# Kernel tuning notes

Measured on AMD Instinct MI355X. Metric: run time of the kernel, lower is better.

The kernel has to match this reference:

```python
import jax, jax.numpy as jnp
import numpy as np

NUM_HEADS = 16
B, S, D_MODEL = 8, 2048, 1024
HEAD_DIM = 64  # key_dim == value_dim == D_MODEL // NUM_HEADS


def setup_inputs() -> dict:
    key = jax.random.key(0)
    ks = jax.random.split(key, 8)
    s_in = 1.0 / np.sqrt(D_MODEL)
    s_out = 1.0 / np.sqrt(NUM_HEADS * HEAD_DIM)
    return {
        "query": jax.random.normal(ks[0], (B, S, D_MODEL), jnp.float32),
        "key": jax.random.normal(ks[1], (B, S, D_MODEL), jnp.float32),
        "value": jax.random.normal(ks[2], (B, S, D_MODEL), jnp.float32),
        "Wq": jax.random.normal(ks[3], (D_MODEL, HEAD_DIM), jnp.float32) * s_in,
        "bq": jnp.zeros((HEAD_DIM,), jnp.float32),
        "Wk": jax.random.normal(ks[4], (D_MODEL, HEAD_DIM), jnp.float32) * s_in,
        "bk": jnp.zeros((HEAD_DIM,), jnp.float32),
        "Wv": jax.random.normal(ks[5], (D_MODEL, HEAD_DIM), jnp.float32) * s_in,
        "bv": jnp.zeros((HEAD_DIM,), jnp.float32),
        "Wo": jax.random.normal(ks[6], (NUM_HEADS * HEAD_DIM, D_MODEL), jnp.float32) * s_out,
        "bo": jnp.zeros((D_MODEL,), jnp.float32),
    }


def reference(query, key, value, Wq, bq, Wk, bk, Wv, bv, Wo, bo):
    # Projections (same Linear reused for every "head" in the original code)
    q = query @ Wq + bq   # [B, S, head_dim]
    k = key @ Wk + bk     # [B, S, head_dim]
    v = value @ Wv + bv   # [B, S, head_dim]
    scale = jnp.sqrt(jnp.asarray(q.shape[-1], q.dtype))
    scores = jnp.einsum("bqd,bkd->bqk", q, k) / scale  # [B, S, S]
    attn = jax.nn.softmax(scores, axis=-1)
    ctx = jnp.einsum("bqk,bkd->bqd", attn, v)          # [B, S, head_dim]
    # All num_heads outputs are identical -> concat == tile
    cat = jnp.tile(ctx, (1, 1, NUM_HEADS))             # [B, S, num_heads*head_dim]
    return cat @ Wo + bo                               # [B, S, D_MODEL]
```

## Files before the change

### kernel.cpp

```cpp
#include <hip/hip_runtime.h>


typedef __attribute__((ext_vector_type(8))) unsigned short ushort8v;

__device__ __forceinline__ float bf2f(unsigned short u) {
    unsigned int x = ((unsigned int)u) << 16;
    return __builtin_bit_cast(float, x);
}

__device__ __forceinline__ bool detect_bf16(const void* p, int nwords) {
    const unsigned short* w = (const unsigned short*)p;
    int sane = 0;
    for (int i = 0; i < nwords; ++i) {
        unsigned e = (w[i] >> 7) & 0xFF;
        sane += (e == 0 || (e >= 0x60 && e <= 0x9F)) ? 1 : 0;
    }
    return sane * 10 >= nwords * 9;
}

__device__ __forceinline__ float load_in(const void* p, long idx, bool isbf16) {
    return isbf16 ? bf2f(((const unsigned short*)p)[idx]) : ((const float*)p)[idx];
}

__global__ __launch_bounds__(256) void prep_wosum(const void* __restrict__ Wo,
                                                  float* __restrict__ wosum) {
    __shared__ bool fwb;
    if (threadIdx.x == 0) fwb = detect_bf16(Wo, 256);
    __syncthreads();
    bool wb = fwb;
    int id = blockIdx.x * 256 + threadIdx.x;
    int d = id >> 10, n = id & 1023;
    float s = 0.f;
#pragma unroll
    for (int h = 0; h < 16; ++h) s += load_in(Wo, (long)(h * 64 + d) * 1024 + n, wb);
    wosum[id] = s;
}

__global__ __launch_bounds__(256) void proj_t(
    const void* __restrict__ X0, const void* __restrict__ X1, const void* __restrict__ X2,
    const void* __restrict__ bq, const void* __restrict__ bk, const void* __restrict__ bv,
    const void* __restrict__ Wq, const void* __restrict__ Wk, const void* __restrict__ Wv,
    float* __restrict__ qo, float* __restrict__ ko, float* __restrict__ vo) {
    int p = blockIdx.y;
    const void* X    = (p == 0) ? X0 : (p == 1) ? X1 : X2;
    const void* W    = (p == 0) ? Wq : (p == 1) ? Wk : Wv;
    const void* bias = (p == 0) ? bq : (p == 1) ? bk : bv;
    float* out       = (p == 0) ? qo : (p == 1) ? ko : vo;

    __shared__ bool fxb, fwb, fbb;
    __shared__ __align__(16) float Xt[64 * 68];
    __shared__ __align__(16) float Ws[64 * 68];
    if (threadIdx.x == 0) {
        fxb = detect_bf16(X, 256);
        fwb = detect_bf16(W, 256);
        fbb = detect_bf16(bias, 64);
    }
    __syncthreads();
    const bool xb = fxb, wb = fwb, bb = fbb;

    const int t = threadIdx.x;
    const long row0 = (long)blockIdx.x * 64;
    const int row4 = (t >> 4) * 4;
    const int col4 = (t & 15) * 4;
    const int sr0 = (t >> 4) * 4;
    const int sk4 = (t & 15) * 4;
    const int wk  = t >> 2;
    const int wc0 = (t & 3) * 16;

    float acc[4][4] = {};

    for (int k0 = 0; k0 < 1024; k0 += 64) {
        if (xb) {
            const unsigned short* xp =
                (const unsigned short*)X + (row0 + sr0) * 1024 + k0 + sk4;
            ushort4 u0 = *(const ushort4*)(xp);
            ushort4 u1 = *(const ushort4*)(xp + 1024);
            ushort4 u2 = *(const ushort4*)(xp + 2048);
            ushort4 u3 = *(const ushort4*)(xp + 3072);
            *(float4*)&Xt[(sk4 + 0) * 68 + sr0] =
                make_float4(bf2f(u0.x), bf2f(u1.x), bf2f(u2.x), bf2f(u3.x));
            *(float4*)&Xt[(sk4 + 1) * 68 + sr0] =
                make_float4(bf2f(u0.y), bf2f(u1.y), bf2f(u2.y), bf2f(u3.y));
            *(float4*)&Xt[(sk4 + 2) * 68 + sr0] =
                make_float4(bf2f(u0.z), bf2f(u1.z), bf2f(u2.z), bf2f(u3.z));
            *(float4*)&Xt[(sk4 + 3) * 68 + sr0] =
                make_float4(bf2f(u0.w), bf2f(u1.w), bf2f(u2.w), bf2f(u3.w));
        } else {
            const float* xp = (const float*)X + (row0 + sr0) * 1024 + k0 + sk4;
            float4 a0 = *(const float4*)(xp);
            float4 a1 = *(const float4*)(xp + 1024);
            float4 a2 = *(const float4*)(xp + 2048);
            float4 a3 = *(const float4*)(xp + 3072);
            *(float4*)&Xt[(sk4 + 0) * 68 + sr0] = make_float4(a0.x, a1.x, a2.x, a3.x);
            *(float4*)&Xt[(sk4 + 1) * 68 + sr0] = make_float4(a0.y, a1.y, a2.y, a3.y);
            *(float4*)&Xt[(sk4 + 2) * 68 + sr0] = make_float4(a0.z, a1.z, a2.z, a3.z);
            *(float4*)&Xt[(sk4 + 3) * 68 + sr0] = make_float4(a0.w, a1.w, a2.w, a3.w);
        }
        if (wb) {
            const unsigned short* wp =
                (const unsigned short*)W + (long)(k0 + wk) * 64 + wc0;
            ushort8v u0 = *(const ushort8v*)(wp);
            ushort8v u1 = *(const ushort8v*)(wp + 8);
            float* wd = &Ws[wk * 68 + wc0];
            *(float4*)(wd + 0)  = make_float4(bf2f(u0[0]), bf2f(u0[1]), bf2f(u0[2]), bf2f(u0[3]));
            *(float4*)(wd + 4)  = make_float4(bf2f(u0[4]), bf2f(u0[5]), bf2f(u0[6]), bf2f(u0[7]));
            *(float4*)(wd + 8)  = make_float4(bf2f(u1[0]), bf2f(u1[1]), bf2f(u1[2]), bf2f(u1[3]));
            *(float4*)(wd + 12) = make_float4(bf2f(u1[4]), bf2f(u1[5]), bf2f(u1[6]), bf2f(u1[7]));
        } else {
            const float* wp = (const float*)W + (long)(k0 + wk) * 64 + wc0;
            float* wd = &Ws[wk * 68 + wc0];
            *(float4*)(wd + 0)  = *(const float4*)(wp + 0);
            *(float4*)(wd + 4)  = *(const float4*)(wp + 4);
            *(float4*)(wd + 8)  = *(const float4*)(wp + 8);
            *(float4*)(wd + 12) = *(const float4*)(wp + 12);
        }
        __syncthreads();

#pragma unroll 4
        for (int kk = 0; kk < 64; ++kk) {
            float4 xv = *(const float4*)&Xt[kk * 68 + row4];
            float4 wv = *(const float4*)&Ws[kk * 68 + col4];
            float xa[4] = {xv.x, xv.y, xv.z, xv.w};
            float wa[4] = {wv.x, wv.y, wv.z, wv.w};
#pragma unroll
            for (int i = 0; i < 4; ++i)
#pragma unroll
                for (int j = 0; j < 4; ++j) acc[i][j] += xa[i] * wa[j];
        }
        __syncthreads();
    }

    float b0 = load_in(bias, col4 + 0, bb);
    float b1 = load_in(bias, col4 + 1, bb);
    float b2 = load_in(bias, col4 + 2, bb);
    float b3 = load_in(bias, col4 + 3, bb);
#pragma unroll
    for (int i = 0; i < 4; ++i)
        *(float4*)&out[(row0 + row4 + i) * 64 + col4] =
            make_float4(acc[i][0] + b0, acc[i][1] + b1, acc[i][2] + b2, acc[i][3] + b3);
}

__global__ __launch_bounds__(256) void attn_t(const float* __restrict__ q,
                                              const float* __restrict__ k,
                                              const float* __restrict__ v,
                                              float* __restrict__ ctx) {
    const int b = blockIdx.y;
    const long kvbase = (long)b * 2048;
    const long qbase  = kvbase + (long)blockIdx.x * 64;

    __shared__ __align__(16) float Qt[64 * 68];
    __shared__ __align__(16) float Kt[64 * 68];
    __shared__ __align__(16) float Pt[64 * 68];

    const int tid = threadIdx.x;
    const int qg4 = (tid >> 4) * 4;
    const int g16 = tid & 15;
    const int kg4 = g16 * 4;
    const int dg4 = g16 * 4;
    const int sr0 = (tid >> 4) * 4;
    const int sd4 = (tid & 15) * 4;

    {
        const float* qp = &q[(qbase + sr0) * 64 + sd4];
        float4 a0 = *(const float4*)(qp);
        float4 a1 = *(const float4*)(qp + 64);
        float4 a2 = *(const float4*)(qp + 128);
        float4 a3 = *(const float4*)(qp + 192);
        const float sc = 0.125f;
        *(float4*)&Qt[(sd4 + 0) * 68 + sr0] = make_float4(a0.x * sc, a1.x * sc, a2.x * sc, a3.x * sc);
        *(float4*)&Qt[(sd4 + 1) * 68 + sr0] = make_float4(a0.y * sc, a1.y * sc, a2.y * sc, a3.y * sc);
        *(float4*)&Qt[(sd4 + 2) * 68 + sr0] = make_float4(a0.z * sc, a1.z * sc, a2.z * sc, a3.z * sc);
        *(float4*)&Qt[(sd4 + 3) * 68 + sr0] = make_float4(a0.w * sc, a1.w * sc, a2.w * sc, a3.w * sc);
    }

    float o[4][4] = {};
    float m[4] = {-INFINITY, -INFINITY, -INFINITY, -INFINITY};
    float l[4] = {};

    for (int t0 = 0; t0 < 2048; t0 += 64) {
        {
            const float* kp = &k[(kvbase + t0 + sr0) * 64 + sd4];
            float4 a0 = *(const float4*)(kp);
            float4 a1 = *(const float4*)(kp + 64);
            float4 a2 = *(const float4*)(kp + 128);
            float4 a3 = *(const float4*)(kp + 192);
            *(float4*)&Kt[(sd4 + 0) * 68 + sr0] = make_float4(a0.x, a1.x, a2.x, a3.x);
            *(float4*)&Kt[(sd4 + 1) * 68 + sr0] = make_float4(a0.y, a1.y, a2.y, a3.y);
            *(float4*)&Kt[(sd4 + 2) * 68 + sr0] = make_float4(a0.z, a1.z, a2.z, a3.z);
            *(float4*)&Kt[(sd4 + 3) * 68 + sr0] = make_float4(a0.w, a1.w, a2.w, a3.w);
        }
        __syncthreads();

        float s[4][4] = {};
#pragma unroll 4
        for (int d = 0; d < 64; ++d) {
            float4 qv = *(const float4*)&Qt[d * 68 + qg4];
            float4 kv = *(const float4*)&Kt[d * 68 + kg4];
            float qa[4] = {qv.x, qv.y, qv.z, qv.w};
            float ka[4] = {kv.x, kv.y, kv.z, kv.w};
#pragma unroll
            for (int qi = 0; qi < 4; ++qi)
#pragma unroll
                for (int kj = 0; kj < 4; ++kj) s[qi][kj] += qa[qi] * ka[kj];
        }

#pragma unroll
        for (int qi = 0; qi < 4; ++qi) {
            float pm = fmaxf(fmaxf(s[qi][0], s[qi][1]), fmaxf(s[qi][2], s[qi][3]));
            pm = fmaxf(pm, __shfl_xor(pm, 1));
            pm = fmaxf(pm, __shfl_xor(pm, 2));
            pm = fmaxf(pm, __shfl_xor(pm, 4));
            pm = fmaxf(pm, __shfl_xor(pm, 8));
            float mn = fmaxf(m[qi], pm);
            float f = __expf(m[qi] - mn);
            m[qi] = mn;
            float ts = 0.f;
#pragma unroll
            for (int kj = 0; kj < 4; ++kj) {
                float pv = __expf(s[qi][kj] - mn);
                s[qi][kj] = pv;
                ts += pv;
            }
            ts += __shfl_xor(ts, 1);
            ts += __shfl_xor(ts, 2);
            ts += __shfl_xor(ts, 4);
            ts += __shfl_xor(ts, 8);
            l[qi] = l[qi] * f + ts;
#pragma unroll
            for (int di = 0; di < 4; ++di) o[qi][di] *= f;
        }

#pragma unroll
        for (int kj = 0; kj < 4; ++kj)
            *(float4*)&Pt[(kg4 + kj) * 68 + qg4] = make_float4(s[0][kj], s[1][kj], s[2][kj], s[3][kj]);
        __syncthreads();

        const float* vb = &v[(kvbase + t0) * 64 + dg4];
#pragma unroll 4
        for (int kk = 0; kk < 64; ++kk) {
            float4 p4 = *(const float4*)&Pt[kk * 68 + qg4];
            float4 v4 = *(const float4*)&vb[kk * 64];
            float pa[4] = {p4.x, p4.y, p4.z, p4.w};
            float va[4] = {v4.x, v4.y, v4.z, v4.w};
#pragma unroll
            for (int qi = 0; qi < 4; ++qi)
#pragma unroll
                for (int di = 0; di < 4; ++di) o[qi][di] += pa[qi] * va[di];
        }
    }

#pragma unroll
    for (int qi = 0; qi < 4; ++qi) {
        float inv = 1.f / l[qi];
        *(float4*)&ctx[(qbase + qg4 + qi) * 64 + dg4] =
            make_float4(o[qi][0] * inv, o[qi][1] * inv, o[qi][2] * inv, o[qi][3] * inv);
    }
}

__global__ __launch_bounds__(256) void out_t(const float* __restrict__ ctx,
                                             const float* __restrict__ wosum,
                                             const void* __restrict__ bo,
                                             float* __restrict__ out) {
    __shared__ __align__(16) float cr[8 * 64];
    __shared__ bool fbb;
    int t = threadIdx.x;
    long row0 = (long)blockIdx.x * 8;
    if (t == 0) fbb = detect_bf16(bo, 256);
    if (t < 128) {
        int r = t >> 4, d4 = (t & 15) * 4;
        *(float4*)&cr[r * 64 + d4] = *(const float4*)&ctx[(row0 + r) * 64 + d4];
    }
    __syncthreads();
    bool bob = fbb;
    int c = t * 4;
    float a[8][4];
    {
        float b0 = load_in(bo, c + 0, bob), b1 = load_in(bo, c + 1, bob);
        float b2 = load_in(bo, c + 2, bob), b3 = load_in(bo, c + 3, bob);
#pragma unroll
        for (int r = 0; r < 8; ++r) { a[r][0] = b0; a[r][1] = b1; a[r][2] = b2; a[r][3] = b3; }
    }
#pragma unroll 4
    for (int d = 0; d < 64; ++d) {
        float4 w4 = *(const float4*)&wosum[d * 1024 + c];
#pragma unroll
        for (int r = 0; r < 8; ++r) {
            float cv = cr[r * 64 + d];
            a[r][0] += cv * w4.x;
            a[r][1] += cv * w4.y;
            a[r][2] += cv * w4.z;
            a[r][3] += cv * w4.w;
        }
    }
#pragma unroll
    for (int r = 0; r < 8; ++r)
        *(float4*)&out[(row0 + r) * 1024 + c] = make_float4(a[r][0], a[r][1], a[r][2], a[r][3]);
}

extern "C" void kernel_launch(void* const* d_in, const int* in_sizes, int n_in,
                              void* d_out, int out_size, void* d_ws, size_t ws_size,
                              hipStream_t stream) {
    const void* big[3] = {0, 0, 0};  int nbig = 0;
    const void* w64k[3] = {0, 0, 0}; int nw = 0;
    const void* b64[3] = {0, 0, 0};  int nb = 0;
    const void* Wo = 0; const void* bo = 0;
    for (int i = 0; i < n_in; ++i) {
        int s = in_sizes[i];
        if (s == 16777216 && nbig < 3)     big[nbig++] = d_in[i];
        else if (s == 65536 && nw < 3)     w64k[nw++] = d_in[i];
        else if (s == 64 && nb < 3)        b64[nb++] = d_in[i];
        else if (s == 1048576)             Wo = d_in[i];
        else if (s == 1024)                bo = d_in[i];
    }
    const void* query = big[0]  ? big[0]  : d_in[0];
    const void* key   = big[1]  ? big[1]  : d_in[1];
    const void* value = big[2]  ? big[2]  : d_in[2];
    const void* Wq    = w64k[0] ? w64k[0] : d_in[3];
    const void* Wk    = w64k[1] ? w64k[1] : d_in[5];
    const void* Wv    = w64k[2] ? w64k[2] : d_in[7];
    const void* bq    = b64[0]  ? b64[0]  : d_in[4];
    const void* bk    = b64[1]  ? b64[1]  : d_in[6];
    const void* bv    = b64[2]  ? b64[2]  : d_in[8];
    if (!Wo) Wo = d_in[9];
    if (!bo) bo = d_in[10];
    float* out = (float*)d_out;

    char* ws = (char*)d_ws;
    float* wosum = (float*)(ws);
    float* q     = (float*)(ws + 1048576);
    float* k     = (float*)(ws + 1048576 + 4194304);
    float* v     = (float*)(ws + 1048576 + 2*4194304);
    float* ctx   = (float*)(ws + 1048576 + 3*4194304);

    hipLaunchKernelGGL(prep_wosum, dim3(256),       dim3(256), 0, stream, Wo, wosum);
    hipLaunchKernelGGL(proj_t,     dim3(256, 3),    dim3(256), 0, stream,
                       query, key, value, bq, bk, bv, Wq, Wk, Wv, q, k, v);
    hipLaunchKernelGGL(attn_t,     dim3(32, 8),     dim3(256), 0, stream, q, k, v, ctx);
    hipLaunchKernelGGL(out_t,      dim3(2048),      dim3(256), 0, stream, ctx, wosum, bo, out);
}
```

Measured before the change: 621.2 us.

## Split attention over keys with merge kernel, smaller query tiles, prefetch tiles

The attention kernel now handles 32 queries per block instead of 64 and optionally splits the key range across two blocks (split-K flash decoding), writing partial outputs plus max and sum that a new merge kernel combines. This raises the block count from 256 to 1024, so the GPU's many CUs are better occupied. K tiles and the projection GEMM tiles are now register-prefetched one step ahead to overlap global loads with compute. In exchange it adds a merge pass, extra workspace traffic for partials, and a dependency on workspace size.

```diff
diff --git a/kernel.cpp b/kernel.cpp
--- a/kernel.cpp
+++ b/kernel.cpp
@@ -67,55 +67,77 @@
     const int wk  = t >> 2;
     const int wc0 = (t & 3) * 16;
 
-    float acc[4][4] = {};
-
-    for (int k0 = 0; k0 < 1024; k0 += 64) {
+    ushort4 xu0, xu1, xu2, xu3;
+    float4  xf0, xf1, xf2, xf3;
+    ushort8v wu0, wu1;
+    float4  wf0, wf1, wf2, wf3;
+
+    auto loadTile = [&](int k0) {
         if (xb) {
             const unsigned short* xp =
                 (const unsigned short*)X + (row0 + sr0) * 1024 + k0 + sk4;
-            ushort4 u0 = *(const ushort4*)(xp);
-            ushort4 u1 = *(const ushort4*)(xp + 1024);
-            ushort4 u2 = *(const ushort4*)(xp + 2048);
-            ushort4 u3 = *(const ushort4*)(xp + 3072);
-            *(float4*)&Xt[(sk4 + 0) * 68 + sr0] =
-                make_float4(bf2f(u0.x), bf2f(u1.x), bf2f(u2.x), bf2f(u3.x));
-            *(float4*)&Xt[(sk4 + 1) * 68 + sr0] =
-                make_float4(bf2f(u0.y), bf2f(u1.y), bf2f(u2.y), bf2f(u3.y));
-            *(float4*)&Xt[(sk4 + 2) * 68 + sr0] =
-                make_float4(bf2f(u0.z), bf2f(u1.z), bf2f(u2.z), bf2f(u3.z));
-            *(float4*)&Xt[(sk4 + 3) * 68 + sr0] =
-                make_float4(bf2f(u0.w), bf2f(u1.w), bf2f(u2.w), bf2f(u3.w));
+            xu0 = *(const ushort4*)(xp);
+            xu1 = *(const ushort4*)(xp + 1024);
+            xu2 = *(const ushort4*)(xp + 2048);
+            xu3 = *(const ushort4*)(xp + 3072);
         } else {
             const float* xp = (const float*)X + (row0 + sr0) * 1024 + k0 + sk4;
-            float4 a0 = *(const float4*)(xp);
-            float4 a1 = *(const float4*)(xp + 1024);
-            float4 a2 = *(const float4*)(xp + 2048);
-            float4 a3 = *(const float4*)(xp + 3072);
-            *(float4*)&Xt[(sk4 + 0) * 68 + sr0] = make_float4(a0.x, a1.x, a2.x, a3.x);
-            *(float4*)&Xt[(sk4 + 1) * 68 + sr0] = make_float4(a0.y, a1.y, a2.y, a3.y);
-            *(float4*)&Xt[(sk4 + 2) * 68 + sr0] = make_float4(a0.z, a1.z, a2.z, a3.z);
-            *(float4*)&Xt[(sk4 + 3) * 68 + sr0] = make_float4(a0.w, a1.w, a2.w, a3.w);
+            xf0 = *(const float4*)(xp);
+            xf1 = *(const float4*)(xp + 1024);
+            xf2 = *(const float4*)(xp + 2048);
+            xf3 = *(const float4*)(xp + 3072);
         }
         if (wb) {
             const unsigned short* wp =
                 (const unsigned short*)W + (long)(k0 + wk) * 64 + wc0;
-            ushort8v u0 = *(const ushort8v*)(wp);
-            ushort8v u1 = *(const ushort8v*)(wp + 8);
-            float* wd = &Ws[wk * 68 + wc0];
-            *(float4*)(wd + 0)  = make_float4(bf2f(u0[0]), bf2f(u0[1]), bf2f(u0[2]), bf2f(u0[3]));
-            *(float4*)(wd + 4)  = make_float4(bf2f(u0[4]), bf2f(u0[5]), bf2f(u0[6]), bf2f(u0[7]));
-            *(float4*)(wd + 8)  = make_float4(bf2f(u1[0]), bf2f(u1[1]), bf2f(u1[2]), bf2f(u1[3]));
-            *(float4*)(wd + 12) = make_float4(bf2f(u1[4]), bf2f(u1[5]), bf2f(u1[6]), bf2f(u1[7]));
+            wu0 = *(const ushort8v*)(wp);
+            wu1 = *(const ushort8v*)(wp + 8);
         } else {
             const float* wp = (const float*)W + (long)(k0 + wk) * 64 + wc0;
-            float* wd = &Ws[wk * 68 + wc0];
-            *(float4*)(wd + 0)  = *(const float4*)(wp + 0);
-            *(float4*)(wd + 4)  = *(const float4*)(wp + 4);
-            *(float4*)(wd + 8)  = *(const float4*)(wp + 8);
-            *(float4*)(wd + 12) = *(const float4*)(wp + 12);
-        }
-        __syncthreads();
-
+            wf0 = *(const float4*)(wp + 0);
+            wf1 = *(const float4*)(wp + 4);
+            wf2 = *(const float4*)(wp + 8);
+            wf3 = *(const float4*)(wp + 12);
+        }
+    };
+    auto writeTile = [&]() {
+        if (xb) {
+            *(float4*)&Xt[(sk4 + 0) * 68 + sr0] =
+                make_float4(bf2f(xu0.x), bf2f(xu1.x), bf2f(xu2.x), bf2f(xu3.x));
+            *(float4*)&Xt[(sk4 + 1) * 68 + sr0] =
+                make_float4(bf2f(xu0.y), bf2f(xu1.y), bf2f(xu2.y), bf2f(xu3.y));
+            *(float4*)&Xt[(sk4 + 2) * 68 + sr0] =
+                make_float4(bf2f(xu0.z), bf2f(xu1.z), bf2f(xu2.z), bf2f(xu3.z));
+            *(float4*)&Xt[(sk4 + 3) * 68 + sr0] =
+                make_float4(bf2f(xu0.w), bf2f(xu1.w), bf2f(xu2.w), bf2f(xu3.w));
+        } else {
+            *(float4*)&Xt[(sk4 + 0) * 68 + sr0] = make_float4(xf0.x, xf1.x, xf2.x, xf3.x);
+            *(float4*)&Xt[(sk4 + 1) * 68 + sr0] = make_float4(xf0.y, xf1.y, xf2.y, xf3.y);
+            *(float4*)&Xt[(sk4 + 2) * 68 + sr0] = make_float4(xf0.z, xf1.z, xf2.z, xf3.z);
+            *(float4*)&Xt[(sk4 + 3) * 68 + sr0] = make_float4(xf0.w, xf1.w, xf2.w, xf3.w);
+        }
+        float* wd = &Ws[wk * 68 + wc0];
+        if (wb) {
+            *(float4*)(wd + 0)  = make_float4(bf2f(wu0[0]), bf2f(wu0[1]), bf2f(wu0[2]), bf2f(wu0[3]));
+            *(float4*)(wd + 4)  = make_float4(bf2f(wu0[4]), bf2f(wu0[5]), bf2f(wu0[6]), bf2f(wu0[7]));
+            *(float4*)(wd + 8)  = make_float4(bf2f(wu1[0]), bf2f(wu1[1]), bf2f(wu1[2]), bf2f(wu1[3]));
+            *(float4*)(wd + 12) = make_float4(bf2f(wu1[4]), bf2f(wu1[5]), bf2f(wu1[6]), bf2f(wu1[7]));
+        } else {
+            *(float4*)(wd + 0)  = wf0;
+            *(float4*)(wd + 4)  = wf1;
+            *(float4*)(wd + 8)  = wf2;
+            *(float4*)(wd + 12) = wf3;
+        }
+    };
+
+    loadTile(0);
+    writeTile();
+    __syncthreads();
+
+    float acc[4][4] = {};
+    for (int k0 = 0; k0 < 1024; k0 += 64) {
+        const bool more = (k0 + 64 < 1024);
+        if (more) loadTile(k0 + 64);
 #pragma unroll 4
         for (int kk = 0; kk < 64; ++kk) {
             float4 xv = *(const float4*)&Xt[kk * 68 + row4];
@@ -127,7 +149,11 @@
 #pragma unroll
                 for (int j = 0; j < 4; ++j) acc[i][j] += xa[i] * wa[j];
         }
-        __syncthreads();
+        if (more) {
+            __syncthreads();
+            writeTile();
+            __syncthreads();
+        }
     }
 
     float b0 = load_in(bias, col4 + 0, bb);
@@ -140,78 +166,97 @@
             make_float4(acc[i][0] + b0, acc[i][1] + b1, acc[i][2] + b2, acc[i][3] + b3);
 }
 
-__global__ __launch_bounds__(256) void attn_t(const float* __restrict__ q,
+__global__ __launch_bounds__(256) void attn_p(const float* __restrict__ q,
                                               const float* __restrict__ k,
                                               const float* __restrict__ v,
-                                              float* __restrict__ ctx) {
+                                              float* __restrict__ ctx,
+                                              float* __restrict__ po,
+                                              float* __restrict__ pm,
+                                              float* __restrict__ pl,
+                                              int ns) {
     const int b = blockIdx.y;
+    const int qt = blockIdx.x;
+    const int split = blockIdx.z;
+    const int keys = 2048 / ns;
+    const int NT = keys >> 6;
     const long kvbase = (long)b * 2048;
-    const long qbase  = kvbase + (long)blockIdx.x * 64;
-
-    __shared__ __align__(16) float Qt[64 * 68];
+    const long qbase  = kvbase + (long)qt * 32;
+    const long kstart = kvbase + (long)split * keys;
+
+    __shared__ __align__(16) float Qt[64 * 36];
     __shared__ __align__(16) float Kt[64 * 68];
-    __shared__ __align__(16) float Pt[64 * 68];
+    __shared__ __align__(16) float Pt[64 * 36];
 
     const int tid = threadIdx.x;
-    const int qg4 = (tid >> 4) * 4;
     const int g16 = tid & 15;
+    const int qg2 = (tid >> 4) * 2;
     const int kg4 = g16 * 4;
     const int dg4 = g16 * 4;
-    const int sr0 = (tid >> 4) * 4;
-    const int sd4 = (tid & 15) * 4;
-
-    {
-        const float* qp = &q[(qbase + sr0) * 64 + sd4];
+    const int skr = (tid >> 4) * 4;
+    const int skd = g16 * 4;
+
+    if (tid < 128) {
+        const int sqr = (tid >> 4) * 4;
+        const int sqd = (tid & 15) * 4;
+        const float* qp = &q[(qbase + sqr) * 64 + sqd];
         float4 a0 = *(const float4*)(qp);
         float4 a1 = *(const float4*)(qp + 64);
         float4 a2 = *(const float4*)(qp + 128);
         float4 a3 = *(const float4*)(qp + 192);
         const float sc = 0.125f;
-        *(float4*)&Qt[(sd4 + 0) * 68 + sr0] = make_float4(a0.x * sc, a1.x * sc, a2.x * sc, a3.x * sc);
-        *(float4*)&Qt[(sd4 + 1) * 68 + sr0] = make_float4(a0.y * sc, a1.y * sc, a2.y * sc, a3.y * sc);
-        *(float4*)&Qt[(sd4 + 2) * 68 + sr0] = make_float4(a0.z * sc, a1.z * sc, a2.z * sc, a3.z * sc);
-        *(float4*)&Qt[(sd4 + 3) * 68 + sr0] = make_float4(a0.w * sc, a1.w * sc, a2.w * sc, a3.w * sc);
-    }
-
-    float o[4][4] = {};
-    float m[4] = {-INFINITY, -INFINITY, -INFINITY, -INFINITY};
-    float l[4] = {};
-
-    for (int t0 = 0; t0 < 2048; t0 += 64) {
-        {
-            const float* kp = &k[(kvbase + t0 + sr0) * 64 + sd4];
-            float4 a0 = *(const float4*)(kp);
-            float4 a1 = *(const float4*)(kp + 64);
-            float4 a2 = *(const float4*)(kp + 128);
-            float4 a3 = *(const float4*)(kp + 192);
-            *(float4*)&Kt[(sd4 + 0) * 68 + sr0] = make_float4(a0.x, a1.x, a2.x, a3.x);
-            *(float4*)&Kt[(sd4 + 1) * 68 + sr0] = make_float4(a0.y, a1.y, a2.y, a3.y);
-            *(float4*)&Kt[(sd4 + 2) * 68 + sr0] = make_float4(a0.z, a1.z, a2.z, a3.z);
-            *(float4*)&Kt[(sd4 + 3) * 68 + sr0] = make_float4(a0.w, a1.w, a2.w, a3.w);
-        }
-        __syncthreads();
-
-        float s[4][4] = {};
+        *(float4*)&Qt[(sqd + 0) * 36 + sqr] = make_float4(a0.x * sc, a1.x * sc, a2.x * sc, a3.x * sc);
+        *(float4*)&Qt[(sqd + 1) * 36 + sqr] = make_float4(a0.y * sc, a1.y * sc, a2.y * sc, a3.y * sc);
+        *(float4*)&Qt[(sqd + 2) * 36 + sqr] = make_float4(a0.z * sc, a1.z * sc, a2.z * sc, a3.z * sc);
+        *(float4*)&Qt[(sqd + 3) * 36 + sqr] = make_float4(a0.w * sc, a1.w * sc, a2.w * sc, a3.w * sc);
+    }
+
+    float4 ka0, ka1, ka2, ka3;
+    auto loadK = [&](int t1) {
+        const float* kp = &k[(kstart + t1 * 64 + skr) * 64 + skd];
+        ka0 = *(const float4*)(kp);
+        ka1 = *(const float4*)(kp + 64);
+        ka2 = *(const float4*)(kp + 128);
+        ka3 = *(const float4*)(kp + 192);
+    };
+    auto writeK = [&]() {
+        *(float4*)&Kt[(skd + 0) * 68 + skr] = make_float4(ka0.x, ka1.x, ka2.x, ka3.x);
+        *(float4*)&Kt[(skd + 1) * 68 + skr] = make_float4(ka0.y, ka1.y, ka2.y, ka3.y);
+        *(float4*)&Kt[(skd + 2) * 68 + skr] = make_float4(ka0.z, ka1.z, ka2.z, ka3.z);
+        *(float4*)&Kt[(skd + 3) * 68 + skr] = make_float4(ka0.w, ka1.w, ka2.w, ka3.w);
+    };
+
+    loadK(0);
+    writeK();
+    __syncthreads();
+
+    float o[2][4] = {};
+    float m[2] = {-INFINITY, -INFINITY};
+    float l[2] = {};
+
+    for (int t1 = 0; t1 < NT; ++t1) {
+        if (t1 + 1 < NT) loadK(t1 + 1);
+
+        float s[2][4] = {};
 #pragma unroll 4
         for (int d = 0; d < 64; ++d) {
-            float4 qv = *(const float4*)&Qt[d * 68 + qg4];
+            float2 qv = *(const float2*)&Qt[d * 36 + qg2];
             float4 kv = *(const float4*)&Kt[d * 68 + kg4];
-            float qa[4] = {qv.x, qv.y, qv.z, qv.w};
             float ka[4] = {kv.x, kv.y, kv.z, kv.w};
 #pragma unroll
-            for (int qi = 0; qi < 4; ++qi)
-#pragma unroll
-                for (int kj = 0; kj < 4; ++kj) s[qi][kj] += qa[qi] * ka[kj];
-        }
-
-#pragma unroll
-        for (int qi = 0; qi < 4; ++qi) {
-            float pm = fmaxf(fmaxf(s[qi][0], s[qi][1]), fmaxf(s[qi][2], s[qi][3]));
-            pm = fmaxf(pm, __shfl_xor(pm, 1));
-            pm = fmaxf(pm, __shfl_xor(pm, 2));
-            pm = fmaxf(pm, __shfl_xor(pm, 4));
-            pm = fmaxf(pm, __shfl_xor(pm, 8));
-            float mn = fmaxf(m[qi], pm);
+            for (int kj = 0; kj < 4; ++kj) {
+                s[0][kj] += qv.x * ka[kj];
+                s[1][kj] += qv.y * ka[kj];
+            }
+        }
+
+#pragma unroll
+        for (int qi = 0; qi < 2; ++qi) {
+            float pmx = fmaxf(fmaxf(s[qi][0], s[qi][1]), fmaxf(s[qi][2], s[qi][3]));
+            pmx = fmaxf(pmx, __shfl_xor(pmx, 1));
+            pmx = fmaxf(pmx, __shfl_xor(pmx, 2));
+            pmx = fmaxf(pmx, __shfl_xor(pmx, 4));
+            pmx = fmaxf(pmx, __shfl_xor(pmx, 8));
+            float mn = fmaxf(m[qi], pmx);
             float f = __expf(m[qi] - mn);
             m[qi] = mn;
             float ts = 0.f;
@@ -232,29 +277,71 @@
 
 #pragma unroll
         for (int kj = 0; kj < 4; ++kj)
-            *(float4*)&Pt[(kg4 + kj) * 68 + qg4] = make_float4(s[0][kj], s[1][kj], s[2][kj], s[3][kj]);
+            *(float2*)&Pt[(kg4 + kj) * 36 + qg2] = make_float2(s[0][kj], s[1][kj]);
         __syncthreads();
 
-        const float* vb = &v[(kvbase + t0) * 64 + dg4];
+        const float* vb = &v[(kstart + t1 * 64) * 64 + dg4];
 #pragma unroll 4
         for (int kk = 0; kk < 64; ++kk) {
-            float4 p4 = *(const float4*)&Pt[kk * 68 + qg4];
+            float2 p2 = *(const float2*)&Pt[kk * 36 + qg2];
             float4 v4 = *(const float4*)&vb[kk * 64];
-            float pa[4] = {p4.x, p4.y, p4.z, p4.w};
             float va[4] = {v4.x, v4.y, v4.z, v4.w};
 #pragma unroll
-            for (int qi = 0; qi < 4; ++qi)
-#pragma unroll
-                for (int di = 0; di < 4; ++di) o[qi][di] += pa[qi] * va[di];
-        }
-    }
-
-#pragma unroll
-    for (int qi = 0; qi < 4; ++qi) {
-        float inv = 1.f / l[qi];
-        *(float4*)&ctx[(qbase + qg4 + qi) * 64 + dg4] =
-            make_float4(o[qi][0] * inv, o[qi][1] * inv, o[qi][2] * inv, o[qi][3] * inv);
-    }
+            for (int di = 0; di < 4; ++di) {
+                o[0][di] += p2.x * va[di];
+                o[1][di] += p2.y * va[di];
+            }
+        }
+
+        if (t1 + 1 < NT) writeK();
+        __syncthreads();
+    }
+
+    if (ns == 1) {
+#pragma unroll
+        for (int qi = 0; qi < 2; ++qi) {
+            float inv = 1.f / l[qi];
+            *(float4*)&ctx[(qbase + qg2 + qi) * 64 + dg4] =
+                make_float4(o[qi][0] * inv, o[qi][1] * inv, o[qi][2] * inv, o[qi][3] * inv);
+        }
+    } else {
+        const long idx = (long)(b * 64 + qt) * ns + split;
+#pragma unroll
+        for (int qi = 0; qi < 2; ++qi)
+            *(float4*)&po[idx * 2048 + (qg2 + qi) * 64 + dg4] =
+                make_float4(o[qi][0], o[qi][1], o[qi][2], o[qi][3]);
+        if (g16 == 0) {
+#pragma unroll
+            for (int qi = 0; qi < 2; ++qi) {
+                pm[idx * 32 + qg2 + qi] = m[qi];
+                pl[idx * 32 + qg2 + qi] = l[qi];
+            }
+        }
+    }
+}
+
+__global__ __launch_bounds__(256) void attn_merge(const float* __restrict__ po,
+                                                  const float* __restrict__ pm,
+                                                  const float* __restrict__ pl,
+                                                  float* __restrict__ ctx,
+                                                  int ns) {
+    const int t = threadIdx.x;
+    const long r = (long)blockIdx.x * 4 + (t >> 6);
+    const int d = t & 63;
+    const int b = (int)(r >> 11);
+    const int rr = (int)(r & 2047);
+    const int qt = rr >> 5;
+    const int rloc = rr & 31;
+    const long base = (long)(b * 64 + qt) * ns;
+    float M = -INFINITY;
+    for (int s = 0; s < ns; ++s) M = fmaxf(M, pm[(base + s) * 32 + rloc]);
+    float L = 0.f, num = 0.f;
+    for (int s = 0; s < ns; ++s) {
+        float e = __expf(pm[(base + s) * 32 + rloc] - M);
+        L += pl[(base + s) * 32 + rloc] * e;
+        num += po[(base + s) * 2048 + rloc * 64 + d] * e;
+    }
+    ctx[r * 64 + d] = num / L;
 }
 
 __global__ __launch_bounds__(256) void out_t(const float* __restrict__ ctx,
@@ -331,10 +418,18 @@
     float* k     = (float*)(ws + 1048576 + 4194304);
     float* v     = (float*)(ws + 1048576 + 2*4194304);
     float* ctx   = (float*)(ws + 1048576 + 3*4194304);
-
-    hipLaunchKernelGGL(prep_wosum, dim3(256),       dim3(256), 0, stream, Wo, wosum);
-    hipLaunchKernelGGL(proj_t,     dim3(256, 3),    dim3(256), 0, stream,
+    const size_t PO_OFF = 1048576 + (size_t)4 * 4194304;
+    int ns = (ws_size >= PO_OFF + 2 * 4194304ull + 2 * 131072ull) ? 2 : 1;
+    float* po = (float*)(ws + PO_OFF);
+    float* pm = (float*)(ws + PO_OFF + (size_t)ns * 4194304);
+    float* pl = pm + (size_t)ns * 16384;
+
+    hipLaunchKernelGGL(prep_wosum, dim3(256),        dim3(256), 0, stream, Wo, wosum);
+    hipLaunchKernelGGL(proj_t,     dim3(256, 3),     dim3(256), 0, stream,
                        query, key, value, bq, bk, bv, Wq, Wk, Wv, q, k, v);
-    hipLaunchKernelGGL(attn_t,     dim3(32, 8),     dim3(256), 0, stream, q, k, v, ctx);
-    hipLaunchKernelGGL(out_t,      dim3(2048),      dim3(256), 0, stream, ctx, wosum, bo, out);
-}
+    hipLaunchKernelGGL(attn_p,     dim3(64, 8, ns),  dim3(256), 0, stream,
+                       q, k, v, ctx, po, pm, pl, ns);
+    if (ns > 1)
+        hipLaunchKernelGGL(attn_merge, dim3(4096),   dim3(256), 0, stream, po, pm, pl, ctx, ns);
+    hipLaunchKernelGGL(out_t,      dim3(2048),       dim3(256), 0, stream, ctx, wosum, bo, out);
+}
```

Measured after the change: 544.2 us. 12.4% less time.
